# Kernel tuning notes

Measured on AMD Instinct MI355X. Metric: run time of the kernel, lower is better.

The kernel has to match this reference:

```python
import jax, jax.numpy as jnp
import numpy as np

NUM_CLASSES = 80
C_OUT = 81
SCORE_THR = 0.02
IOU_THR = 0.45
TOPK = 1000
IMG_MAX = 320.0
STRIDES = [16, 32, 64, 107, 160, 320]
MIN_SIZES = [48, 100, 150, 202, 253, 304]
MAX_SIZES = [100, 150, 202, 253, 304, 320]
FEAT = [20, 10, 5, 3, 2, 1]
MAX_RATIO = float(abs(np.log(0.016)))


def _base_anchors(level):
    base = float(MIN_SIZES[level])
    scales = np.array([1.0, np.sqrt(MAX_SIZES[level] / MIN_SIZES[level])])
    ratios = np.array([1.0, 0.5, 2.0, 1.0 / 3.0, 3.0])
    h_ratios = np.sqrt(ratios)
    w_ratios = 1.0 / h_ratios
    # scale_major=False: scales vary along rows
    ws = (base * scales[:, None] * w_ratios[None, :]).reshape(-1)
    hs = (base * scales[:, None] * h_ratios[None, :]).reshape(-1)
    c = STRIDES[level] / 2.0
    ba = np.stack([c - 0.5 * ws, c - 0.5 * hs, c + 0.5 * ws, c + 0.5 * hs], -1)
    return ba[[0, 5, 1, 2, 3, 4]]  # index_select reorder, 6 anchors/loc


def _priors(level):
    ba = _base_anchors(level)
    f, s = FEAT[level], STRIDES[level]
    sx = np.arange(f, dtype=np.float64) * s
    xx = np.tile(sx, f)
    yy = np.repeat(sx, f)
    shifts = np.stack([xx, yy, xx, yy], -1)  # [f*f,4]
    return (ba[None, :, :] + shifts[:, None, :]).reshape(-1, 4).astype(np.float32)


PRIORS = [jnp.asarray(_priors(i)) for i in range(6)]


def delta2bbox(priors, deltas):
    stds = jnp.array([0.1, 0.1, 0.2, 0.2], dtype=deltas.dtype)
    d = deltas * stds
    pxy = (priors[:, :2] + priors[:, 2:]) * 0.5
    pwh = priors[:, 2:] - priors[:, :2]
    dwh = jnp.clip(d[:, 2:], -MAX_RATIO, MAX_RATIO)
    gxy = pxy + pwh * d[:, :2]
    gwh = pwh * jnp.exp(dwh)
    boxes = jnp.concatenate([gxy - 0.5 * gwh, gxy + 0.5 * gwh], -1)
    return jnp.clip(boxes, 0.0, IMG_MAX)


def _nms_keep(boxes, valid, iou_thr):
    # greedy NMS over score-sorted boxes; returns bool keep mask
    K = boxes.shape[0]
    area = (boxes[:, 2] - boxes[:, 0]) * (boxes[:, 3] - boxes[:, 1])
    lt = jnp.maximum(boxes[:, None, :2], boxes[None, :, :2])
    rb = jnp.minimum(boxes[:, None, 2:], boxes[None, :, 2:])
    wh = jnp.clip(rb - lt, 0.0)
    inter = wh[..., 0] * wh[..., 1]
    iou = inter / (area[:, None] + area[None, :] - inter)
    ar = jnp.arange(K)

    def body(i, alive):
        sup = (iou[i] > iou_thr) & (ar > i) & alive[i]
        return alive & ~sup

    return jax.lax.fori_loop(0, K, body, valid)


def _single_image(cls_list, bb_list):
    boxes_l, scores_l, labels_l, valid_l = [], [], [], []
    for cls, bb, priors in zip(cls_list, bb_list, PRIORS):
        probs = jax.nn.softmax(cls.transpose(1, 2, 0).reshape(-1, C_OUT), axis=-1)[:, :NUM_CLASSES]
        flat = probs.reshape(-1)  # [N*80]
        k = min(TOPK, flat.shape[0])
        masked = jnp.where(flat > SCORE_THR, flat, -1.0)
        vals, idx = jax.lax.top_k(masked, k)
        valid = vals > SCORE_THR
        a_idx = idx // NUM_CLASSES
        lbl = idx % NUM_CLASSES
        deltas = bb.transpose(1, 2, 0).reshape(-1, 4)[a_idx]
        boxes = delta2bbox(priors[a_idx], deltas)
        boxes_l.append(boxes)
        scores_l.append(jnp.where(valid, vals, 0.0))
        labels_l.append(lbl)
        valid_l.append(valid)
    boxes = jnp.concatenate(boxes_l, 0)   # [K,4]
    scores = jnp.concatenate(scores_l, 0)
    labels = jnp.concatenate(labels_l, 0)
    valid = jnp.concatenate(valid_l, 0)

    # batched (class-aware) NMS via per-class coordinate offsets
    max_coord = boxes.max()
    offsets = labels.astype(boxes.dtype) * (max_coord + 1.0)
    boxes_nms = boxes + offsets[:, None]
    order = jnp.argsort(-jnp.where(valid, scores, -jnp.inf))
    boxes_s = boxes[order]
    scores_s = scores[order]
    labels_s = labels[order]
    valid_s = valid[order]
    keep = jax.lax.stop_gradient(
        _nms_keep(jax.lax.stop_gradient(boxes_nms[order]), valid_s, IOU_THR))
    dets = jnp.concatenate([boxes_s, scores_s[:, None]], -1) * keep[:, None].astype(boxes.dtype)
    return dets, labels_s, keep


def setup_inputs() -> dict:
    key = jax.random.key(0)
    ks = jax.random.split(key, 12)
    B = 4
    inp = {}
    for i, f in enumerate(FEAT):
        inp[f"cls{i}"] = jax.random.normal(ks[i], (B, 486, f, f), dtype=jnp.float32)
        inp[f"bb{i}"] = jax.random.normal(ks[6 + i], (B, 24, f, f), dtype=jnp.float32)
    return inp


def reference(cls0, cls1, cls2, cls3, cls4, cls5, bb0, bb1, bb2, bb3, bb4, bb5):
    def one(c0, c1, c2, c3, c4, c5, b0, b1, b2, b3, b4, b5):
        return _single_image([c0, c1, c2, c3, c4, c5], [b0, b1, b2, b3, b4, b5])
    dets, labels, keep = jax.vmap(one)(cls0, cls1, cls2, cls3, cls4, cls5,
                                       bb0, bb1, bb2, bb3, bb4, bb5)
    return dets, labels, keep
```

## Files before the change

### kernel.cpp

```cpp
#include <hip/hip_runtime.h>
#include <stdint.h>

#define NB 4
#define KTOT 5480
#define PER_IMG 258720
#define SCORE_THR 0.02f
#define IOU_THR 0.45f
#define REL_BASE 0x3CA3D70Bu
#define JCH 10
#define JSZ 548
#define ICH 11
#define NMSCAP 512

__constant__ int cFEAT[6]    = {20,10,5,3,2,1};
__constant__ int cSTRIDE[6]  = {16,32,64,107,160,320};
__constant__ int cMIN[6]     = {48,100,150,202,253,304};
__constant__ int cMAX[6]     = {100,150,202,253,304,320};
__constant__ int cNFLAT[6]   = {192000,48000,12000,4320,1920,480};
__constant__ int cFLATOFF[6] = {0,192000,240000,252000,256320,258240};
__constant__ int cKSEL[6]    = {1000,1000,1000,1000,1000,480};
__constant__ int cKOFF[6]    = {0,1000,2000,3000,4000,5000};
__constant__ double cRATIO[6] = {1.0,1.0,0.5,2.0,1.0/3.0,3.0};
__constant__ int eTLEV[14]   = {0,0,0,0,0,0,0,0,1,1,2,3,4,5};
__constant__ int eTCHK[14]   = {0,1,2,3,4,5,6,7,0,1,0,0,0,0};
__constant__ int eNCH[6]     = {8,2,1,1,1,1};

__device__ __forceinline__ unsigned long long mk_key(unsigned kb, int lev, unsigned idx) {
  return ((unsigned long long)kb << 21) |
         (unsigned long long)(0x1FFFFFu ^ (((unsigned)lev << 18) | idx));
}

__device__ __forceinline__ unsigned long long shfl64(unsigned long long x, int src) {
  int lo = __shfl((int)(unsigned)(x & 0xffffffffull), src);
  int hi = __shfl((int)(unsigned)(x >> 32), src);
  return ((unsigned long long)(unsigned)hi << 32) | (unsigned)lo;
}

__global__ __launch_bounds__(256) void k_softmax(
    const float* __restrict__ c0, const float* __restrict__ c1,
    const float* __restrict__ c2, const float* __restrict__ c3,
    const float* __restrict__ c4, const float* __restrict__ c5,
    float* __restrict__ scores, unsigned* __restrict__ ghist)
{
  int t = blockIdx.x;
  int b = t / 78, rem = t % 78;
  int lev, a, cb;
  if (rem < 42)      { lev = 0; a = rem / 7;        cb = (rem % 7) * 64; }
  else if (rem < 54) { lev = 1; a = (rem - 42) >> 1; cb = ((rem - 42) & 1) * 64; }
  else               { lev = 2 + (rem - 54) / 6; a = (rem - 54) % 6; cb = 0; }
  const float* cls = (lev==0)?c0:(lev==1)?c1:(lev==2)?c2:(lev==3)?c3:(lev==4)?c4:c5;
  int f = cFEAT[lev], ff = f * f;
  int ncell = ff - cb; if (ncell > 64) ncell = 64;

  __shared__ float tile[81 * 64];
  const float* base = cls + (size_t)(b * 486 + a * 81) * ff + cb;
  for (int t2 = threadIdx.x; t2 < 81 * 64; t2 += 256) {
    int c = t2 >> 6, cell = t2 & 63;
    if (cell < ncell)
      tile[(c << 6) | (cell ^ (c & 63))] = base[c * ff + cell];
  }
  __syncthreads();

  int lane = threadIdx.x & 63, w = threadIdx.x >> 6;
  unsigned* h = ghist + (size_t)(b * 6 + lev) * 8192;
  for (int cell = w; cell < ncell; cell += 4) {
    float v1 = tile[(lane << 6) | (cell ^ lane)];
    float v2 = (lane <= 16) ? tile[((lane + 64) << 6) | (cell ^ lane)]
                            : __uint_as_float(0xff800000u);
    float mx = fmaxf(v1, v2);
    #pragma unroll
    for (int m = 32; m; m >>= 1) mx = fmaxf(mx, __shfl_xor(mx, m));
    float e1 = expf(v1 - mx);
    float e2 = (lane <= 16) ? expf(v2 - mx) : 0.f;
    float sm = e1 + e2;
    #pragma unroll
    for (int m = 32; m; m >>= 1) sm += __shfl_xor(sm, m);
    int row = (cb + cell) * 6 + a;
    float* out = scores + (size_t)b * PER_IMG + cFLATOFF[lev] + row * 80;
    float p1 = e1 / sm;
    out[lane] = (p1 > SCORE_THR) ? p1 : -1.f;
    if (p1 > SCORE_THR)
      atomicAdd(&h[(__float_as_uint(p1) - REL_BASE) >> 13], 1u);
    if (lane < 16) {
      float p2 = e2 / sm;
      out[lane + 64] = (p2 > SCORE_THR) ? p2 : -1.f;
      if (p2 > SCORE_THR)
        atomicAdd(&h[(__float_as_uint(p2) - REL_BASE) >> 13], 1u);
    }
  }
}

__global__ __launch_bounds__(1024) void k_plan(
    const unsigned* __restrict__ ghist, unsigned* __restrict__ ctrl)
{
  int task = blockIdx.x;
  int lev = task % 6;
  int tid = threadIdx.x;
  if (lev == 5) { if (tid == 0) ctrl[task * 8] = 2u; return; }
  unsigned k = (unsigned)cKSEL[lev];
  const unsigned* h = ghist + (size_t)task * 8192;
  unsigned loc[8];
  unsigned ssum = 0;
  #pragma unroll
  for (int j = 0; j < 8; ++j) { loc[j] = h[tid * 8 + j]; ssum += loc[j]; }
  __shared__ unsigned sc[1024];
  sc[tid] = ssum;
  __syncthreads();
  for (int off = 1; off < 1024; off <<= 1) {
    unsigned cur = sc[tid];
    unsigned add = (tid + off < 1024) ? sc[tid + off] : 0u;
    __syncthreads();
    sc[tid] = cur + add;
    __syncthreads();
  }
  unsigned c = sc[0];
  if (c < k) { if (tid == 0) ctrl[task * 8] = 1u; return; }
  unsigned above = (tid == 1023) ? 0u : sc[tid + 1];
  unsigned run = above;
  #pragma unroll
  for (int j = 7; j >= 0; --j) {
    unsigned hj = loc[j];
    if (run < k && run + hj >= k) {
      ctrl[task * 8 + 0] = 0u;
      ctrl[task * 8 + 1] = (unsigned)(tid * 8 + j);
    }
    run += hj;
  }
}

__global__ __launch_bounds__(256) void k_emit2(
    const float* __restrict__ scores, unsigned* __restrict__ ctrl,
    unsigned long long* __restrict__ selkeys, unsigned long long* __restrict__ eqg)
{
  int b = blockIdx.x / 14, ent = blockIdx.x % 14;
  int lev = eTLEV[ent], chk = eTCHK[ent];
  int task = b * 6 + lev;
  int n = cNFLAT[lev];
  int tid = threadIdx.x;
  const float* s = scores + (size_t)b * PER_IMG + cFLATOFF[lev];
  unsigned long long* out = selkeys + (size_t)b * KTOT + cKOFF[lev];

  if (lev == 5) {
    for (int i = tid; i < n; i += 256) {
      float v = s[i];
      unsigned kb = (v > SCORE_THR) ? __float_as_uint(v) : 0u;
      out[i] = mk_key(kb, lev, (unsigned)i);
    }
    return;
  }

  __shared__ unsigned long long wbuf[1024];
  __shared__ unsigned long long ebuf[4096];
  __shared__ unsigned wcnt, ecnt, sbw, sbe;
  if (tid == 0) { wcnt = 0; ecnt = 0; }
  __syncthreads();

  unsigned mode = ctrl[task * 8];
  int csz = n / eNCH[lev];
  int start = chk * csz;
  const float4* s4 = (const float4*)(s + start);
  int n4 = csz >> 2;

  if (mode == 0u) {
    unsigned b1 = ctrl[task * 8 + 1];
    unsigned base_lo = REL_BASE + (b1 << 13);
    unsigned base_hi = base_lo + 8192u;
    #pragma unroll 4
    for (int i0 = tid; i0 < n4; i0 += 256) {
      float4 vv = s4[i0];
      #pragma unroll
      for (int e2 = 0; e2 < 4; ++e2) {
        float v = (e2==0)?vv.x:(e2==1)?vv.y:(e2==2)?vv.z:vv.w;
        if (v > SCORE_THR) {
          unsigned kb = __float_as_uint(v);
          unsigned idx = (unsigned)(start + i0 * 4 + e2);
          if (kb >= base_hi) {
            unsigned p = atomicAdd(&wcnt, 1u);
            if (p < 1024u) wbuf[p] = mk_key(kb, lev, idx);
          } else if (kb >= base_lo) {
            unsigned p = atomicAdd(&ecnt, 1u);
            if (p < 4096u) ebuf[p] = mk_key(kb, lev, idx);
          }
        }
      }
    }
  } else {
    #pragma unroll 4
    for (int i0 = tid; i0 < n4; i0 += 256) {
      float4 vv = s4[i0];
      #pragma unroll
      for (int e2 = 0; e2 < 4; ++e2) {
        float v = (e2==0)?vv.x:(e2==1)?vv.y:(e2==2)?vv.z:vv.w;
        if (v > SCORE_THR) {
          unsigned p = atomicAdd(&wcnt, 1u);
          if (p < 1024u) wbuf[p] = mk_key(__float_as_uint(v), lev,
                                          (unsigned)(start + i0 * 4 + e2));
        }
      }
    }
  }
  __syncthreads();
  if (tid == 0) {
    sbw = atomicAdd(&ctrl[task * 8 + 2], wcnt);
    sbe = atomicAdd(&ctrl[task * 8 + 3], ecnt);
  }
  __syncthreads();
  unsigned nw = (wcnt < 1024u) ? wcnt : 1024u;
  unsigned ne = (ecnt < 4096u) ? ecnt : 4096u;
  unsigned bw = sbw, be = sbe;
  for (unsigned t = tid; t < nw; t += 256) out[bw + t] = wbuf[t];
  for (unsigned t = tid; t < ne; t += 256) {
    unsigned g = be + t;
    if (g < 4096u) eqg[(size_t)task * 4096 + g] = ebuf[t];
  }
}

__global__ __launch_bounds__(1024) void k_finalize2(
    const float* __restrict__ scores, const unsigned* __restrict__ ctrl,
    unsigned long long* __restrict__ selkeys, const unsigned long long* __restrict__ eqg)
{
  int task = blockIdx.x;
  int b = task / 6, lev = task % 6;
  if (lev == 5) return;
  int tid = threadIdx.x;
  unsigned k = (unsigned)cKSEL[lev];
  int n = cNFLAT[lev];
  const float* s = scores + (size_t)b * PER_IMG + cFLATOFF[lev];
  unsigned long long* out = selkeys + (size_t)b * KTOT + cKOFF[lev];
  unsigned levtag = (unsigned)lev << 18;
  unsigned mode = ctrl[task * 8];

  __shared__ unsigned long long eqb[4096];
  __shared__ unsigned sc[1024];
  __shared__ unsigned sh_cnt, sh_eq, sh_byte, sh_r;

  if (mode == 0u) {
    unsigned cnt = ctrl[task * 8 + 2];
    unsigned e = ctrl[task * 8 + 3];
    unsigned need = k - cnt;
    if (e <= 4096u) {
      const unsigned long long* eq = eqg + (size_t)task * 4096;
      if (e == need) {
        for (unsigned t = tid; t < need; t += 1024) out[cnt + t] = eq[t];
        return;
      }
      unsigned P = 1; while (P < e) P <<= 1;
      for (unsigned t = tid; t < P; t += 1024) eqb[t] = (t < e) ? eq[t] : 0ull;
      __syncthreads();
      for (unsigned sz = 2; sz <= P; sz <<= 1)
        for (unsigned st = sz >> 1; st; st >>= 1) {
          for (unsigned w = tid; w < P / 2; w += 1024) {
            unsigned i = ((w & ~(st - 1)) << 1) | (w & (st - 1));
            unsigned l = i | st;
            bool up = ((i & sz) == 0);
            unsigned long long A = eqb[i], B = eqb[l];
            if ((A < B) == up) { eqb[i] = B; eqb[l] = A; }
          }
          __syncthreads();
        }
      for (unsigned t = tid; t < need; t += 1024) out[cnt + t] = eqb[t];
      return;
    }
  } else if (mode == 1u) {
    unsigned c = ctrl[task * 8 + 2];
    unsigned need = k - c;
    unsigned base = 0;
    for (int start = 0; start < n && base < need; start += 1024) {
      int i = start + tid;
      unsigned pred = (i < n && !(s[i] > SCORE_THR)) ? 1u : 0u;
      sc[tid] = pred;
      __syncthreads();
      for (int off = 1; off < 1024; off <<= 1) {
        unsigned add = (tid >= off) ? sc[tid - off] : 0u;
        unsigned v = sc[tid];
        __syncthreads();
        sc[tid] = v + add;
        __syncthreads();
      }
      unsigned incl = sc[tid];
      unsigned total = sc[1023];
      unsigned excl = incl - pred;
      if (pred && (base + excl) < need)
        out[c + base + excl] =
            (unsigned long long)(0x1FFFFFu ^ (levtag | (unsigned)i));
      __syncthreads();
      base += total;
    }
    return;
  }

  unsigned* hist = sc;
  unsigned* equ = (unsigned*)eqb;
  unsigned prefix = 0, r = k;
  for (int pass = 3; pass >= 0; --pass) {
    int shift = pass * 8;
    for (int i = tid; i < 256; i += 1024) hist[i] = 0;
    __syncthreads();
    for (int i = tid; i < n; i += 1024) {
      float v = s[i];
      unsigned kb = (v > SCORE_THR) ? __float_as_uint(v) : 0u;
      bool match = (pass == 3) || (((kb ^ prefix) >> (shift + 8)) == 0u);
      if (match) atomicAdd(&hist[(kb >> shift) & 255u], 1u);
    }
    __syncthreads();
    if (tid == 0) {
      unsigned cum = 0, byte = 0, rr = r;
      for (int bb = 255; bb >= 0; --bb) {
        unsigned hh = hist[bb];
        if (cum + hh >= r) { byte = (unsigned)bb; rr = r - cum; break; }
        cum += hh;
      }
      sh_byte = byte; sh_r = rr;
    }
    __syncthreads();
    prefix |= (sh_byte << shift);
    r = sh_r;
    __syncthreads();
  }
  unsigned Kstar = prefix;
  if (tid == 0) { sh_cnt = 0; sh_eq = 0; }
  __syncthreads();
  for (int i = tid; i < n; i += 1024) {
    float v = s[i];
    unsigned kb = (v > SCORE_THR) ? __float_as_uint(v) : 0u;
    if (kb > Kstar) {
      unsigned slot = atomicAdd(&sh_cnt, 1u);
      out[slot] = mk_key(kb, lev, (unsigned)i);
    } else if (kb == Kstar) {
      unsigned es = atomicAdd(&sh_eq, 1u);
      if (es < 4096u) equ[es] = (unsigned)i;
    }
  }
  __syncthreads();
  unsigned m = sh_cnt;
  unsigned e2 = (sh_eq < 4096u) ? sh_eq : 4096u;
  unsigned need2 = k - m;
  if (e2 > need2) {
    unsigned P = 1; while (P < e2) P <<= 1;
    for (unsigned t = tid; t < P; t += 1024) if (t >= e2) equ[t] = 0xFFFFFFFFu;
    __syncthreads();
    for (unsigned sz = 2; sz <= P; sz <<= 1)
      for (unsigned st = sz >> 1; st; st >>= 1) {
        for (unsigned w = tid; w < P / 2; w += 1024) {
          unsigned i = ((w & ~(st - 1)) << 1) | (w & (st - 1));
          unsigned l = i | st;
          bool up = ((i & sz) == 0);
          unsigned A = equ[i], B = equ[l];
          if ((A > B) == up) { equ[i] = B; equ[l] = A; }
        }
        __syncthreads();
      }
  }
  __syncthreads();
  for (unsigned t = tid; t < need2; t += 1024)
    out[m + t] = ((unsigned long long)Kstar << 21) |
                 (unsigned long long)(0x1FFFFFu ^ (levtag | equ[t]));
}

__global__ __launch_bounds__(512) void k_rank(
    const unsigned long long* __restrict__ selkeys, unsigned* __restrict__ rank_part)
{
  int blk = blockIdx.x;
  int jc = blk % JCH;
  int rest = blk / JCH;
  int ic = rest % ICH, b = rest / ICH;
  int tid = threadIdx.x;
  __shared__ __align__(16) unsigned long long sk[JSZ];
  const unsigned long long* keys = selkeys + (size_t)b * KTOT;
  for (int j = tid; j < JSZ; j += 512) sk[j] = keys[jc * JSZ + j];
  int i = ic * 512 + tid;
  unsigned long long mk = (i < KTOT) ? keys[i] : 0ull;
  __syncthreads();
  unsigned r = 0;
  const ulonglong2* sk2 = (const ulonglong2*)sk;
  #pragma unroll 8
  for (int j = 0; j < JSZ / 2; ++j) {
    ulonglong2 kk = sk2[j];
    r += (kk.x > mk) ? 1u : 0u;
    r += (kk.y > mk) ? 1u : 0u;
  }
  if (i < KTOT) rank_part[((size_t)jc * NB + b) * KTOT + i] = r;
}

__global__ __launch_bounds__(512) void k_decode(
    const unsigned long long* __restrict__ selkeys, const unsigned* __restrict__ rank_part,
    const float* __restrict__ g0, const float* __restrict__ g1,
    const float* __restrict__ g2, const float* __restrict__ g3,
    const float* __restrict__ g4, const float* __restrict__ g5,
    float* __restrict__ boxes, float* __restrict__ oscore,
    unsigned char* __restrict__ lab8, unsigned* __restrict__ obmax_u,
    float* __restrict__ outp)
{
  int b = blockIdx.x / ICH, ic = blockIdx.x % ICH;
  int tid = threadIdx.x;
  int i = ic * 512 + tid;
  __shared__ double ba[6][6][4];
  if (tid < 36) {
    int lev = tid / 6, a = tid % 6;
    double base = (double)cMIN[lev];
    double scl = (a == 1) ? sqrt((double)cMAX[lev] / (double)cMIN[lev]) : 1.0;
    double hr = sqrt(cRATIO[a]);
    double wr = 1.0 / hr;
    double wsz = base * scl * wr;
    double hsz = base * scl * hr;
    double cc = (double)cSTRIDE[lev] / 2.0;
    ba[lev][a][0] = cc - 0.5 * wsz;
    ba[lev][a][1] = cc - 0.5 * hsz;
    ba[lev][a][2] = cc + 0.5 * wsz;
    ba[lev][a][3] = cc + 0.5 * hsz;
  }
  __syncthreads();

  float lmax = 0.f;
  if (i < KTOT) {
    unsigned long long mk = selkeys[(size_t)b * KTOT + i];
    unsigned r = 0;
    #pragma unroll
    for (int jc = 0; jc < JCH; ++jc)
      r += rank_part[((size_t)jc * NB + b) * KTOT + i];
    unsigned tag = 0x1FFFFFu ^ (unsigned)(mk & 0x1FFFFFull);
    int lev = tag >> 18;
    int fi = tag & 0x3FFFF;
    unsigned vb2 = (unsigned)(mk >> 21);
    int valid = (vb2 != 0u);
    float score = valid ? __uint_as_float(vb2) : 0.f;
    int label = fi % 80;
    int arow = fi / 80;
    int a = arow % 6, cell = arow / 6;
    int f = cFEAT[lev], ff = f * f;
    int x = cell % f, y = cell / f;
    const float* gb = (lev==0)?g0:(lev==1)?g1:(lev==2)?g2:(lev==3)?g3:(lev==4)?g4:g5;
    const float* pb = gb + (size_t)(b * 24 + a * 4) * ff + y * f + x;
    float d0 = pb[0] * 0.1f, d1 = pb[ff] * 0.1f;
    float d2 = pb[2 * ff] * 0.2f, d3 = pb[3 * ff] * 0.2f;
    const float MR = (float)4.135166556742356;
    d2 = fminf(fmaxf(d2, -MR), MR);
    d3 = fminf(fmaxf(d3, -MR), MR);
    double shx = (double)(x * cSTRIDE[lev]);
    double shy = (double)(y * cSTRIDE[lev]);
    float p0 = (float)(ba[lev][a][0] + shx);
    float p1 = (float)(ba[lev][a][1] + shy);
    float p2 = (float)(ba[lev][a][2] + shx);
    float p3 = (float)(ba[lev][a][3] + shy);
    float pxc = (p0 + p2) * 0.5f, pyc = (p1 + p3) * 0.5f;
    float pw = p2 - p0, ph = p3 - p1;
    float gx = pxc + pw * d0, gy = pyc + ph * d1;
    float gw = pw * expf(d2), gh = ph * expf(d3);
    float x1 = gx - 0.5f * gw, y1 = gy - 0.5f * gh;
    float x2 = gx + 0.5f * gw, y2 = gy + 0.5f * gh;
    x1 = fminf(fmaxf(x1, 0.f), 320.f);
    y1 = fminf(fmaxf(y1, 0.f), 320.f);
    x2 = fminf(fmaxf(x2, 0.f), 320.f);
    y2 = fminf(fmaxf(y2, 0.f), 320.f);
    size_t o = (size_t)b * KTOT + (size_t)r;
    boxes[o * 4 + 0] = x1; boxes[o * 4 + 1] = y1;
    boxes[o * 4 + 2] = x2; boxes[o * 4 + 3] = y2;
    oscore[o] = score;
    lab8[o] = valid ? (unsigned char)label : (unsigned char)0xFF;
    outp[(size_t)NB * KTOT * 5 + o] = (float)label;
    if (!valid) {
      float* det = outp + o * 5;
      det[0] = 0.f; det[1] = 0.f; det[2] = 0.f; det[3] = 0.f; det[4] = 0.f;
      outp[(size_t)NB * KTOT * 6 + o] = 0.f;
    }
    lmax = fmaxf(fmaxf(x1, y1), fmaxf(x2, y2));
  }
  #pragma unroll
  for (int m = 32; m; m >>= 1) lmax = fmaxf(lmax, __shfl_xor(lmax, m));
  if ((tid & 63) == 0) atomicMax(&obmax_u[b], __float_as_uint(lmax));
}

__global__ __launch_bounds__(256) void k_nms(
    const float* __restrict__ boxes, const float* __restrict__ oscore,
    const unsigned char* __restrict__ lab8, const unsigned* __restrict__ obmax_u,
    float* __restrict__ out)
{
  int blk = blockIdx.x;
  int b = blk / 80, cls = blk % 80;
  int tid = threadIdx.x;
  int lane = tid & 63, w = tid >> 6;

  __shared__ unsigned short list[NMSCAP];
  __shared__ float ox1[NMSCAP], oy1[NMSCAP], ox2[NMSCAP], oy2[NMSCAP];
  __shared__ float oar[NMSCAP], osc[NMSCAP];
  __shared__ float rx1[NMSCAP], ry1[NMSCAP], rx2[NMSCAP], ry2[NMSCAP];
  __shared__ unsigned long long mask[NMSCAP][8];
  __shared__ unsigned ccnt[24], cbase[24];
  __shared__ int sh_n;
  __shared__ unsigned long long alive_s[8];

  float ofs = (float)cls * (__uint_as_float(obmax_u[b]) + 1.0f);
  const unsigned* lb32 = (const unsigned*)(lab8 + (size_t)b * KTOT);

  unsigned long long balA[6][4];
  #pragma unroll
  for (int ci = 0; ci < 6; ++ci) {
    int chunk = w + ci * 4;
    unsigned v = 0xFFFFFFFFu;
    if (chunk < 22) {
      int u = chunk * 64 + lane;
      if (u < KTOT / 4) v = lb32[u];
    }
    unsigned long long m0 = __ballot(((v      ) & 0xFFu) == (unsigned)cls);
    unsigned long long m1 = __ballot(((v >>  8) & 0xFFu) == (unsigned)cls);
    unsigned long long m2 = __ballot(((v >> 16) & 0xFFu) == (unsigned)cls);
    unsigned long long m3 = __ballot(((v >> 24) & 0xFFu) == (unsigned)cls);
    balA[ci][0] = m0; balA[ci][1] = m1; balA[ci][2] = m2; balA[ci][3] = m3;
    if (chunk < 22 && lane == 0)
      ccnt[chunk] = (unsigned)(__popcll(m0) + __popcll(m1) + __popcll(m2) + __popcll(m3));
  }
  __syncthreads();
  if (tid == 0) {
    unsigned tot = 0;
    for (int c = 0; c < 22; ++c) { cbase[c] = tot; tot += ccnt[c]; }
    sh_n = (tot < NMSCAP) ? (int)tot : NMSCAP;
  }
  __syncthreads();
  int n = sh_n;
  unsigned long long blt = (lane == 0) ? 0ull : ((~0ull) >> (64 - lane));
  #pragma unroll
  for (int ci = 0; ci < 6; ++ci) {
    int chunk = w + ci * 4;
    if (chunk < 22) {
      unsigned pos = cbase[chunk];
      unsigned below = (unsigned)(__popcll(balA[ci][0] & blt) + __popcll(balA[ci][1] & blt) +
                                  __popcll(balA[ci][2] & blt) + __popcll(balA[ci][3] & blt));
      unsigned within = 0;
      #pragma unroll
      for (int k = 0; k < 4; ++k) {
        if ((balA[ci][k] >> lane) & 1ull) {
          unsigned mypos = pos + below + within;
          if (mypos < NMSCAP) list[mypos] = (unsigned short)(chunk * 256 + lane * 4 + k);
          ++within;
        }
      }
    }
  }
  __syncthreads();

  for (int t = tid; t < n; t += 256) {
    int pos = list[t];
    size_t o = (size_t)b * KTOT + pos;
    float4 bb = *(const float4*)(boxes + o * 4);
    rx1[t] = bb.x; ry1[t] = bb.y; rx2[t] = bb.z; ry2[t] = bb.w;
    float a1 = bb.x + ofs, b1 = bb.y + ofs, a2 = bb.z + ofs, b2 = bb.w + ofs;
    ox1[t] = a1; oy1[t] = b1; ox2[t] = a2; oy2[t] = b2;
    oar[t] = (a2 - a1) * (b2 - b1);
    osc[t] = oscore[o];
  }
  __syncthreads();

  int nw = (n + 63) >> 6;
  for (int i = tid; i < n; i += 256) {
    float ax1 = ox1[i], ay1 = oy1[i], ax2 = ox2[i], ay2 = oy2[i], aar = oar[i];
    int w0 = i >> 6;
    for (int wd = w0; wd < nw; ++wd) {
      unsigned long long m = 0;
      int jbase = wd << 6;
      int jend = n - jbase; if (jend > 64) jend = 64;
      for (int jj = 0; jj < jend; ++jj) {
        int j = jbase + jj;
        if (j > i) {
          float ix1 = fmaxf(ax1, ox1[j]);
          float iy1 = fmaxf(ay1, oy1[j]);
          float ix2 = fminf(ax2, ox2[j]);
          float iy2 = fminf(ay2, oy2[j]);
          float iw = fmaxf(ix2 - ix1, 0.f);
          float ih = fmaxf(iy2 - iy1, 0.f);
          float inter = iw * ih;
          float iou = inter / (aar + oar[j] - inter);
          if (iou > IOU_THR) m |= (1ull << jj);
        }
      }
      mask[i][wd] = m;
    }
  }
  __syncthreads();

  if (w == 0) {
    unsigned long long aw = 0;
    if (lane < nw) {
      int rem = n - (lane << 6);
      aw = (rem >= 64) ? ~0ull : ((1ull << rem) - 1ull);
    }
    for (int i = 0; i < n; ++i) {
      int wi = i >> 6;
      unsigned long long mrow = (lane >= wi && lane < nw) ? mask[i][lane] : 0ull;
      unsigned long long tw = shfl64(aw, wi);
      if ((tw >> (i & 63)) & 1ull) aw &= ~mrow;
    }
    if (lane < 8) alive_s[lane] = aw;
  }
  __syncthreads();

  for (int t = tid; t < n; t += 256) {
    float kf = ((alive_s[t >> 6] >> (t & 63)) & 1ull) ? 1.f : 0.f;
    int pos = list[t];
    size_t o = (size_t)b * KTOT + pos;
    float* det = out + o * 5;
    det[0] = rx1[t] * kf; det[1] = ry1[t] * kf;
    det[2] = rx2[t] * kf; det[3] = ry2[t] * kf;
    det[4] = osc[t] * kf;
    out[(size_t)NB * KTOT * 6 + o] = kf;
  }
}

extern "C" void kernel_launch(void* const* d_in, const int* in_sizes, int n_in,
                              void* d_out, int out_size, void* d_ws, size_t ws_size,
                              hipStream_t stream) {
  (void)in_sizes; (void)n_in; (void)out_size; (void)ws_size;
  const float* cls[6]; const float* bbx[6];
  for (int i = 0; i < 6; ++i) {
    cls[i] = (const float*)d_in[2 * i];
    bbx[i] = (const float*)d_in[2 * i + 1];
  }
  char* ws = (char*)d_ws;
  float* scores = (float*)ws;
  unsigned* rank_part = (unsigned*)ws;
  unsigned long long* selkeys = (unsigned long long*)(ws + 4139520);
  float* boxes  = (float*)(ws + 4314880);
  float* oscore = (float*)(ws + 4665600);
  unsigned char* lab8 = (unsigned char*)(ws + 4753280);
  unsigned* obmax_u = (unsigned*)(ws + 5016320);
  unsigned* ghist = (unsigned*)(ws + 5016576);
  unsigned* ctrl  = (unsigned*)(ws + 5803008);
  unsigned long long* eqg = (unsigned long long*)(ws + 5803776);

  hipMemsetAsync(ws + 5016320, 0, 787456, stream);
  k_softmax<<<NB * 78, 256, 0, stream>>>(cls[0], cls[1], cls[2], cls[3], cls[4], cls[5],
                                         scores, ghist);
  k_plan<<<24, 1024, 0, stream>>>(ghist, ctrl);
  k_emit2<<<NB * 14, 256, 0, stream>>>(scores, ctrl, selkeys, eqg);
  k_finalize2<<<24, 1024, 0, stream>>>(scores, ctrl, selkeys, eqg);
  k_rank<<<NB * ICH * JCH, 512, 0, stream>>>(selkeys, rank_part);
  k_decode<<<NB * ICH, 512, 0, stream>>>(selkeys, rank_part, bbx[0], bbx[1], bbx[2],
                                         bbx[3], bbx[4], bbx[5], boxes, oscore, lab8,
                                         obmax_u, (float*)d_out);
  k_nms<<<NB * 80, 256, 0, stream>>>(boxes, oscore, lab8, obmax_u, (float*)d_out);
}
```

Measured before the change: 113.2 us.

## Replace global atomic histogram with per-block shared histograms and drop plan kernel

Softmax blocks now build a coarse 512-bin histogram in shared memory and write it out per block, rather than doing global atomics into an 8192-bin histogram. The separate plan kernel and the memset are removed: workspace zeroing moves into block 0 of the softmax kernel, and the emit and finalize kernels each reduce the per-block histograms and compute the threshold bin themselves. This saves two launches and cuts global atomic contention. In exchange the bins are coarser, so more elements may land in the boundary bucket, and the histogram reduction is repeated in each consumer block.

Result: faster. 105.4 us (-6.9%).

```diff
diff --git a/kernel.cpp b/kernel.cpp
--- a/kernel.cpp
+++ b/kernel.cpp
@@ -11,6 +11,7 @@
 #define JSZ 548
 #define ICH 11
 #define NMSCAP 512
+#define HBINS 512
 
 __constant__ int cFEAT[6]    = {20,10,5,3,2,1};
 __constant__ int cSTRIDE[6]  = {16,32,64,107,160,320};
@@ -24,6 +25,8 @@
 __constant__ int eTLEV[14]   = {0,0,0,0,0,0,0,0,1,1,2,3,4,5};
 __constant__ int eTCHK[14]   = {0,1,2,3,4,5,6,7,0,1,0,0,0,0};
 __constant__ int eNCH[6]     = {8,2,1,1,1,1};
+__constant__ int hL0[6]      = {0,42,54,60,66,72};
+__constant__ int hLN[6]      = {42,12,6,6,6,6};
 
 __device__ __forceinline__ unsigned long long mk_key(unsigned kb, int lev, unsigned idx) {
   return ((unsigned long long)kb << 21) |
@@ -40,12 +43,18 @@
     const float* __restrict__ c0, const float* __restrict__ c1,
     const float* __restrict__ c2, const float* __restrict__ c3,
     const float* __restrict__ c4, const float* __restrict__ c5,
-    float* __restrict__ scores, unsigned* __restrict__ ghist)
+    float* __restrict__ scores, unsigned* __restrict__ bhist,
+    unsigned* __restrict__ obmax_u, unsigned* __restrict__ ctrl)
 {
   int t = blockIdx.x;
+  int tid = threadIdx.x;
+  if (t == 0) {
+    if (tid < 4) obmax_u[tid] = 0u;
+    if (tid >= 64 && tid < 256) ctrl[tid - 64] = 0u;
+  }
   int b = t / 78, rem = t % 78;
   int lev, a, cb;
-  if (rem < 42)      { lev = 0; a = rem / 7;        cb = (rem % 7) * 64; }
+  if (rem < 42)      { lev = 0; a = rem / 7;         cb = (rem % 7) * 64; }
   else if (rem < 54) { lev = 1; a = (rem - 42) >> 1; cb = ((rem - 42) & 1) * 64; }
   else               { lev = 2 + (rem - 54) / 6; a = (rem - 54) % 6; cb = 0; }
   const float* cls = (lev==0)?c0:(lev==1)?c1:(lev==2)?c2:(lev==3)?c3:(lev==4)?c4:c5;
@@ -53,16 +62,17 @@
   int ncell = ff - cb; if (ncell > 64) ncell = 64;
 
   __shared__ float tile[81 * 64];
+  __shared__ unsigned hcnt[HBINS];
+  for (int i = tid; i < HBINS; i += 256) hcnt[i] = 0;
   const float* base = cls + (size_t)(b * 486 + a * 81) * ff + cb;
-  for (int t2 = threadIdx.x; t2 < 81 * 64; t2 += 256) {
+  for (int t2 = tid; t2 < 81 * 64; t2 += 256) {
     int c = t2 >> 6, cell = t2 & 63;
     if (cell < ncell)
       tile[(c << 6) | (cell ^ (c & 63))] = base[c * ff + cell];
   }
   __syncthreads();
 
-  int lane = threadIdx.x & 63, w = threadIdx.x >> 6;
-  unsigned* h = ghist + (size_t)(b * 6 + lev) * 8192;
+  int lane = tid & 63, w = tid >> 6;
   for (int cell = w; cell < ncell; cell += 4) {
     float v1 = tile[(lane << 6) | (cell ^ lane)];
     float v2 = (lane <= 16) ? tile[((lane + 64) << 6) | (cell ^ lane)]
@@ -80,57 +90,23 @@
     float p1 = e1 / sm;
     out[lane] = (p1 > SCORE_THR) ? p1 : -1.f;
     if (p1 > SCORE_THR)
-      atomicAdd(&h[(__float_as_uint(p1) - REL_BASE) >> 13], 1u);
+      atomicAdd(&hcnt[(__float_as_uint(p1) - REL_BASE) >> 17], 1u);
     if (lane < 16) {
       float p2 = e2 / sm;
       out[lane + 64] = (p2 > SCORE_THR) ? p2 : -1.f;
       if (p2 > SCORE_THR)
-        atomicAdd(&h[(__float_as_uint(p2) - REL_BASE) >> 13], 1u);
-    }
-  }
-}
-
-__global__ __launch_bounds__(1024) void k_plan(
-    const unsigned* __restrict__ ghist, unsigned* __restrict__ ctrl)
-{
-  int task = blockIdx.x;
-  int lev = task % 6;
-  int tid = threadIdx.x;
-  if (lev == 5) { if (tid == 0) ctrl[task * 8] = 2u; return; }
-  unsigned k = (unsigned)cKSEL[lev];
-  const unsigned* h = ghist + (size_t)task * 8192;
-  unsigned loc[8];
-  unsigned ssum = 0;
-  #pragma unroll
-  for (int j = 0; j < 8; ++j) { loc[j] = h[tid * 8 + j]; ssum += loc[j]; }
-  __shared__ unsigned sc[1024];
-  sc[tid] = ssum;
-  __syncthreads();
-  for (int off = 1; off < 1024; off <<= 1) {
-    unsigned cur = sc[tid];
-    unsigned add = (tid + off < 1024) ? sc[tid + off] : 0u;
-    __syncthreads();
-    sc[tid] = cur + add;
-    __syncthreads();
-  }
-  unsigned c = sc[0];
-  if (c < k) { if (tid == 0) ctrl[task * 8] = 1u; return; }
-  unsigned above = (tid == 1023) ? 0u : sc[tid + 1];
-  unsigned run = above;
-  #pragma unroll
-  for (int j = 7; j >= 0; --j) {
-    unsigned hj = loc[j];
-    if (run < k && run + hj >= k) {
-      ctrl[task * 8 + 0] = 0u;
-      ctrl[task * 8 + 1] = (unsigned)(tid * 8 + j);
-    }
-    run += hj;
-  }
-}
-
-__global__ __launch_bounds__(256) void k_emit2(
-    const float* __restrict__ scores, unsigned* __restrict__ ctrl,
-    unsigned long long* __restrict__ selkeys, unsigned long long* __restrict__ eqg)
+        atomicAdd(&hcnt[(__float_as_uint(p2) - REL_BASE) >> 17], 1u);
+    }
+  }
+  __syncthreads();
+  unsigned* hb = bhist + (size_t)t * HBINS;
+  for (int i = tid; i < HBINS; i += 256) hb[i] = hcnt[i];
+}
+
+__global__ __launch_bounds__(256) void k_emit(
+    const float* __restrict__ scores, const unsigned* __restrict__ bhist,
+    unsigned* __restrict__ ctrl, unsigned long long* __restrict__ selkeys,
+    unsigned long long* __restrict__ eqg)
 {
   int b = blockIdx.x / 14, ent = blockIdx.x % 14;
   int lev = eTLEV[ent], chk = eTCHK[ent];
@@ -149,22 +125,52 @@
     return;
   }
 
+  unsigned k = (unsigned)cKSEL[lev];
   __shared__ unsigned long long wbuf[1024];
   __shared__ unsigned long long ebuf[4096];
-  __shared__ unsigned wcnt, ecnt, sbw, sbe;
-  if (tid == 0) { wcnt = 0; ecnt = 0; }
-  __syncthreads();
-
-  unsigned mode = ctrl[task * 8];
+  __shared__ unsigned sc[256];
+  __shared__ unsigned wcnt, ecnt, sbw, sbe, sh_mode, sh_b1;
+
+  {
+    unsigned h0 = 0, h1 = 0;
+    int hbase = b * 78 + hL0[lev];
+    for (int j = 0; j < hLN[lev]; ++j) {
+      const unsigned* hb = bhist + (size_t)(hbase + j) * HBINS;
+      h0 += hb[2 * tid];
+      h1 += hb[2 * tid + 1];
+    }
+    sc[tid] = h0 + h1;
+    __syncthreads();
+    for (int off = 1; off < 256; off <<= 1) {
+      unsigned cur = sc[tid];
+      unsigned add = (tid + off < 256) ? sc[tid + off] : 0u;
+      __syncthreads();
+      sc[tid] = cur + add;
+      __syncthreads();
+    }
+    unsigned c = sc[0];
+    if (tid == 0 && c < k) sh_mode = 1u;
+    if (c >= k) {
+      unsigned above = (tid == 255) ? 0u : sc[tid + 1];
+      unsigned run = above;
+      if (run < k && run + h1 >= k) { sh_mode = 0u; sh_b1 = (unsigned)(2 * tid + 1); }
+      run += h1;
+      if (run < k && run + h0 >= k) { sh_mode = 0u; sh_b1 = (unsigned)(2 * tid); }
+    }
+    if (tid == 0) { wcnt = 0; ecnt = 0; }
+    __syncthreads();
+  }
+  unsigned mode = sh_mode;
+
   int csz = n / eNCH[lev];
   int start = chk * csz;
   const float4* s4 = (const float4*)(s + start);
   int n4 = csz >> 2;
 
   if (mode == 0u) {
-    unsigned b1 = ctrl[task * 8 + 1];
-    unsigned base_lo = REL_BASE + (b1 << 13);
-    unsigned base_hi = base_lo + 8192u;
+    unsigned b1 = sh_b1;
+    unsigned base_lo = REL_BASE + (b1 << 17);
+    unsigned base_hi = base_lo + (1u << 17);
     #pragma unroll 4
     for (int i0 = tid; i0 < n4; i0 += 256) {
       float4 vv = s4[i0];
@@ -215,9 +221,10 @@
   }
 }
 
-__global__ __launch_bounds__(1024) void k_finalize2(
-    const float* __restrict__ scores, const unsigned* __restrict__ ctrl,
-    unsigned long long* __restrict__ selkeys, const unsigned long long* __restrict__ eqg)
+__global__ __launch_bounds__(1024) void k_finalize(
+    const float* __restrict__ scores, const unsigned* __restrict__ bhist,
+    const unsigned* __restrict__ ctrl, unsigned long long* __restrict__ selkeys,
+    const unsigned long long* __restrict__ eqg)
 {
   int task = blockIdx.x;
   int b = task / 6, lev = task % 6;
@@ -228,11 +235,30 @@
   const float* s = scores + (size_t)b * PER_IMG + cFLATOFF[lev];
   unsigned long long* out = selkeys + (size_t)b * KTOT + cKOFF[lev];
   unsigned levtag = (unsigned)lev << 18;
-  unsigned mode = ctrl[task * 8];
 
   __shared__ unsigned long long eqb[4096];
   __shared__ unsigned sc[1024];
   __shared__ unsigned sh_cnt, sh_eq, sh_byte, sh_r;
+
+  unsigned hval = 0;
+  if (tid < HBINS) {
+    int hbase = b * 78 + hL0[lev];
+    for (int j = 0; j < hLN[lev]; ++j)
+      hval += bhist[(size_t)(hbase + j) * HBINS + tid];
+  }
+  sc[tid] = (tid < HBINS) ? hval : 0u;
+  __syncthreads();
+  for (int off = 1; off < 1024; off <<= 1) {
+    unsigned cur = sc[tid];
+    unsigned add = (tid + off < 1024) ? sc[tid + off] : 0u;
+    __syncthreads();
+    sc[tid] = cur + add;
+    __syncthreads();
+  }
+  unsigned c = sc[0];
+  __syncthreads();
+  unsigned mode = (c >= k) ? 0u : 1u;
+  bool done = false;
 
   if (mode == 0u) {
     unsigned cnt = ctrl[task * 8 + 2];
@@ -242,10 +268,103 @@
       const unsigned long long* eq = eqg + (size_t)task * 4096;
       if (e == need) {
         for (unsigned t = tid; t < need; t += 1024) out[cnt + t] = eq[t];
-        return;
-      }
-      unsigned P = 1; while (P < e) P <<= 1;
-      for (unsigned t = tid; t < P; t += 1024) eqb[t] = (t < e) ? eq[t] : 0ull;
+      } else {
+        unsigned P = 1; while (P < e) P <<= 1;
+        for (unsigned t = tid; t < P; t += 1024) eqb[t] = (t < e) ? eq[t] : 0ull;
+        __syncthreads();
+        for (unsigned sz = 2; sz <= P; sz <<= 1)
+          for (unsigned st = sz >> 1; st; st >>= 1) {
+            for (unsigned w = tid; w < P / 2; w += 1024) {
+              unsigned i = ((w & ~(st - 1)) << 1) | (w & (st - 1));
+              unsigned l = i | st;
+              bool up = ((i & sz) == 0);
+              unsigned long long A = eqb[i], B = eqb[l];
+              if ((A < B) == up) { eqb[i] = B; eqb[l] = A; }
+            }
+            __syncthreads();
+          }
+        for (unsigned t = tid; t < need; t += 1024) out[cnt + t] = eqb[t];
+      }
+      done = true;
+    }
+  } else {
+    unsigned c2 = ctrl[task * 8 + 2];
+    unsigned need = k - c2;
+    unsigned base = 0;
+    for (int start = 0; start < n && base < need; start += 1024) {
+      int i = start + tid;
+      unsigned pred = (i < n && !(s[i] > SCORE_THR)) ? 1u : 0u;
+      sc[tid] = pred;
+      __syncthreads();
+      for (int off = 1; off < 1024; off <<= 1) {
+        unsigned add = (tid >= off) ? sc[tid - off] : 0u;
+        unsigned v = sc[tid];
+        __syncthreads();
+        sc[tid] = v + add;
+        __syncthreads();
+      }
+      unsigned incl = sc[tid];
+      unsigned total = sc[1023];
+      unsigned excl = incl - pred;
+      if (pred && (base + excl) < need)
+        out[c2 + base + excl] =
+            (unsigned long long)(0x1FFFFFu ^ (levtag | (unsigned)i));
+      __syncthreads();
+      base += total;
+    }
+    done = true;
+  }
+
+  if (!done) {
+    unsigned* hist = sc;
+    unsigned* equ = (unsigned*)eqb;
+    unsigned prefix = 0, r = k;
+    for (int pass = 3; pass >= 0; --pass) {
+      int shift = pass * 8;
+      for (int i = tid; i < 256; i += 1024) hist[i] = 0;
+      __syncthreads();
+      for (int i = tid; i < n; i += 1024) {
+        float v = s[i];
+        unsigned kb = (v > SCORE_THR) ? __float_as_uint(v) : 0u;
+        bool match = (pass == 3) || (((kb ^ prefix) >> (shift + 8)) == 0u);
+        if (match) atomicAdd(&hist[(kb >> shift) & 255u], 1u);
+      }
+      __syncthreads();
+      if (tid == 0) {
+        unsigned cum = 0, byte = 0, rr = r;
+        for (int bb = 255; bb >= 0; --bb) {
+          unsigned hh = hist[bb];
+          if (cum + hh >= r) { byte = (unsigned)bb; rr = r - cum; break; }
+          cum += hh;
+        }
+        sh_byte = byte; sh_r = rr;
+      }
+      __syncthreads();
+      prefix |= (sh_byte << shift);
+      r = sh_r;
+      __syncthreads();
+    }
+    unsigned Kstar = prefix;
+    if (tid == 0) { sh_cnt = 0; sh_eq = 0; }
+    __syncthreads();
+    for (int i = tid; i < n; i += 1024) {
+      float v = s[i];
+      unsigned kb = (v > SCORE_THR) ? __float_as_uint(v) : 0u;
+      if (kb > Kstar) {
+        unsigned slot = atomicAdd(&sh_cnt, 1u);
+        out[slot] = mk_key(kb, lev, (unsigned)i);
+      } else if (kb == Kstar) {
+        unsigned es = atomicAdd(&sh_eq, 1u);
+        if (es < 4096u) equ[es] = (unsigned)i;
+      }
+    }
+    __syncthreads();
+    unsigned m = sh_cnt;
+    unsigned e2 = (sh_eq < 4096u) ? sh_eq : 4096u;
+    unsigned need2 = k - m;
+    if (e2 > need2) {
+      unsigned P = 1; while (P < e2) P <<= 1;
+      for (unsigned t = tid; t < P; t += 1024) if (t >= e2) equ[t] = 0xFFFFFFFFu;
       __syncthreads();
       for (unsigned sz = 2; sz <= P; sz <<= 1)
         for (unsigned st = sz >> 1; st; st >>= 1) {
@@ -253,108 +372,17 @@
             unsigned i = ((w & ~(st - 1)) << 1) | (w & (st - 1));
             unsigned l = i | st;
             bool up = ((i & sz) == 0);
-            unsigned long long A = eqb[i], B = eqb[l];
-            if ((A < B) == up) { eqb[i] = B; eqb[l] = A; }
+            unsigned A = equ[i], B = equ[l];
+            if ((A > B) == up) { equ[i] = B; equ[l] = A; }
           }
           __syncthreads();
         }
-      for (unsigned t = tid; t < need; t += 1024) out[cnt + t] = eqb[t];
-      return;
-    }
-  } else if (mode == 1u) {
-    unsigned c = ctrl[task * 8 + 2];
-    unsigned need = k - c;
-    unsigned base = 0;
-    for (int start = 0; start < n && base < need; start += 1024) {
-      int i = start + tid;
-      unsigned pred = (i < n && !(s[i] > SCORE_THR)) ? 1u : 0u;
-      sc[tid] = pred;
-      __syncthreads();
-      for (int off = 1; off < 1024; off <<= 1) {
-        unsigned add = (tid >= off) ? sc[tid - off] : 0u;
-        unsigned v = sc[tid];
-        __syncthreads();
-        sc[tid] = v + add;
-        __syncthreads();
-      }
-      unsigned incl = sc[tid];
-      unsigned total = sc[1023];
-      unsigned excl = incl - pred;
-      if (pred && (base + excl) < need)
-        out[c + base + excl] =
-            (unsigned long long)(0x1FFFFFu ^ (levtag | (unsigned)i));
-      __syncthreads();
-      base += total;
-    }
-    return;
-  }
-
-  unsigned* hist = sc;
-  unsigned* equ = (unsigned*)eqb;
-  unsigned prefix = 0, r = k;
-  for (int pass = 3; pass >= 0; --pass) {
-    int shift = pass * 8;
-    for (int i = tid; i < 256; i += 1024) hist[i] = 0;
+    }
     __syncthreads();
-    for (int i = tid; i < n; i += 1024) {
-      float v = s[i];
-      unsigned kb = (v > SCORE_THR) ? __float_as_uint(v) : 0u;
-      bool match = (pass == 3) || (((kb ^ prefix) >> (shift + 8)) == 0u);
-      if (match) atomicAdd(&hist[(kb >> shift) & 255u], 1u);
-    }
-    __syncthreads();
-    if (tid == 0) {
-      unsigned cum = 0, byte = 0, rr = r;
-      for (int bb = 255; bb >= 0; --bb) {
-        unsigned hh = hist[bb];
-        if (cum + hh >= r) { byte = (unsigned)bb; rr = r - cum; break; }
-        cum += hh;
-      }
-      sh_byte = byte; sh_r = rr;
-    }
-    __syncthreads();
-    prefix |= (sh_byte << shift);
-    r = sh_r;
-    __syncthreads();
-  }
-  unsigned Kstar = prefix;
-  if (tid == 0) { sh_cnt = 0; sh_eq = 0; }
-  __syncthreads();
-  for (int i = tid; i < n; i += 1024) {
-    float v = s[i];
-    unsigned kb = (v > SCORE_THR) ? __float_as_uint(v) : 0u;
-    if (kb > Kstar) {
-      unsigned slot = atomicAdd(&sh_cnt, 1u);
-      out[slot] = mk_key(kb, lev, (unsigned)i);
-    } else if (kb == Kstar) {
-      unsigned es = atomicAdd(&sh_eq, 1u);
-      if (es < 4096u) equ[es] = (unsigned)i;
-    }
-  }
-  __syncthreads();
-  unsigned m = sh_cnt;
-  unsigned e2 = (sh_eq < 4096u) ? sh_eq : 4096u;
-  unsigned need2 = k - m;
-  if (e2 > need2) {
-    unsigned P = 1; while (P < e2) P <<= 1;
-    for (unsigned t = tid; t < P; t += 1024) if (t >= e2) equ[t] = 0xFFFFFFFFu;
-    __syncthreads();
-    for (unsigned sz = 2; sz <= P; sz <<= 1)
-      for (unsigned st = sz >> 1; st; st >>= 1) {
-        for (unsigned w = tid; w < P / 2; w += 1024) {
-          unsigned i = ((w & ~(st - 1)) << 1) | (w & (st - 1));
-          unsigned l = i | st;
-          bool up = ((i & sz) == 0);
-          unsigned A = equ[i], B = equ[l];
-          if ((A > B) == up) { equ[i] = B; equ[l] = A; }
-        }
-        __syncthreads();
-      }
-  }
-  __syncthreads();
-  for (unsigned t = tid; t < need2; t += 1024)
-    out[m + t] = ((unsigned long long)Kstar << 21) |
-                 (unsigned long long)(0x1FFFFFu ^ (levtag | equ[t]));
+    for (unsigned t = tid; t < need2; t += 1024)
+      out[m + t] = ((unsigned long long)Kstar << 21) |
+                   (unsigned long long)(0x1FFFFFu ^ (levtag | equ[t]));
+  }
 }
 
 __global__ __launch_bounds__(512) void k_rank(
@@ -622,16 +650,14 @@
   float* oscore = (float*)(ws + 4665600);
   unsigned char* lab8 = (unsigned char*)(ws + 4753280);
   unsigned* obmax_u = (unsigned*)(ws + 5016320);
-  unsigned* ghist = (unsigned*)(ws + 5016576);
-  unsigned* ctrl  = (unsigned*)(ws + 5803008);
-  unsigned long long* eqg = (unsigned long long*)(ws + 5803776);
-
-  hipMemsetAsync(ws + 5016320, 0, 787456, stream);
+  unsigned* ctrl    = (unsigned*)(ws + 5016576);
+  unsigned* bhist   = (unsigned*)(ws + 5017600);
+  unsigned long long* eqg = (unsigned long long*)(ws + 5656576);
+
   k_softmax<<<NB * 78, 256, 0, stream>>>(cls[0], cls[1], cls[2], cls[3], cls[4], cls[5],
-                                         scores, ghist);
-  k_plan<<<24, 1024, 0, stream>>>(ghist, ctrl);
-  k_emit2<<<NB * 14, 256, 0, stream>>>(scores, ctrl, selkeys, eqg);
-  k_finalize2<<<24, 1024, 0, stream>>>(scores, ctrl, selkeys, eqg);
+                                         scores, bhist, obmax_u, ctrl);
+  k_emit<<<NB * 14, 256, 0, stream>>>(scores, bhist, ctrl, selkeys, eqg);
+  k_finalize<<<24, 1024, 0, stream>>>(scores, bhist, ctrl, selkeys, eqg);
   k_rank<<<NB * ICH * JCH, 512, 0, stream>>>(selkeys, rank_part);
   k_decode<<<NB * ICH, 512, 0, stream>>>(selkeys, rank_part, bbx[0], bbx[1], bbx[2],
                                          bbx[3], bbx[4], bbx[5], boxes, oscore, lab8,
```
